# Optimization experiments

Hardware: AMD Instinct MI355X
Metric: run time of the kernel (lower is better)

Reference implementation:

```python
import jax, jax.numpy as jnp
import numpy as np

PAD = 0
NEG_INF = -1e30

B, P, Q, D = 32, 4096, 64, 128  # batch, passage len, question len, nhid


def setup_inputs() -> dict:
    key = jax.random.key(0)
    k1, k2, k3, k4, k5, k6 = jax.random.split(key, 6)
    return {
        "tensor_H": jax.random.normal(k1, (B, P, D), dtype=jnp.float32),
        "tensor_U": jax.random.normal(k2, (B, Q, D), dtype=jnp.float32),
        "M": jax.random.normal(k3, (B, P, D), dtype=jnp.float32),
        "sentence_word_rep": jax.random.randint(k4, (B, P), 0, 10000, dtype=jnp.int64),
        "W_attn": jax.random.normal(k5, (D, D), dtype=jnp.float32) / np.sqrt(D),
        "W_cls": jax.random.normal(k6, (5 * D, 2), dtype=jnp.float32) / np.sqrt(5 * D),
    }


def reference(tensor_H, tensor_U, M, sentence_word_rep, W_attn, W_cls):
    # Matrix attention (bilinear): S[b,p,q] = h_p^T W u_q  -> (B, P, Q)
    S = jnp.einsum("bpd,de,bqe->bpq", tensor_H, W_attn, tensor_U)
    # context-to-query: softmax over question axis, then bmm with U
    c2q = jnp.einsum("bpq,bqd->bpd", jax.nn.softmax(S, axis=2), tensor_U)
    # query-to-context: softmax over passage axis of row-max, weighted sum of H
    b_attn = jax.nn.softmax(jnp.max(S, axis=2), axis=-1)        # (B, P)
    q2c = jnp.einsum("bp,bpd->bd", b_attn, tensor_H)[:, None, :]  # (B, 1, D) broadcast over P
    # G = [H; c2q; H*c2q; H*q2c] -> (B, P, 4D); G_M = [G; M] -> (B, P, 5D)
    G_M = jnp.concatenate(
        [tensor_H, c2q, tensor_H * c2q, tensor_H * q2c, M], axis=2
    )
    # masked max-pool over passage positions (mask where token == PAD)
    pad_mask = (sentence_word_rep == PAD)[:, :, None]           # (B, P, 1)
    pooled = jnp.max(jnp.where(pad_mask, NEG_INF, G_M), axis=1)  # (B, 5D)
    # final linear classifier (no bias)
    return pooled @ W_cls                                        # (B, 2)
```

## Files before the change

kernel.cpp:

```cpp
#include <hip/hip_runtime.h>

#define B_ 32
#define P_ 4096
#define Q_ 64
#define D_ 128

#define PART_STRIDE 772
#define NCHUNK 32
#define CHUNK_ROWS 128
#define TWS_BYTES (96*16384)

typedef __attribute__((ext_vector_type(8))) short bf16x8;
typedef __attribute__((ext_vector_type(4))) float f32x4;

__device__ __forceinline__ unsigned int asu(float x) { return __float_as_uint(x); }
__device__ __forceinline__ float asf(unsigned int x) { return __uint_as_float(x); }

__global__ __launch_bounds__(256) void k_T(const float* __restrict__ U,
                                           const float* __restrict__ W,
                                           char* __restrict__ Tws) {
  __shared__ float Wl[128*132];
  __shared__ float Ul[8*128];
  const int b = blockIdx.x >> 3, qc = blockIdx.x & 7;
  const int t = threadIdx.x;
#pragma unroll
  for (int k = 0; k < 16; ++k) {
    int i = t*4 + k*1024;
    float4 wv = *(const float4*)(W + i);
    int d = i >> 7, e = i & 127;
    *(float4*)(&Wl[d*132 + e]) = wv;
  }
  {
    int i = t*4;
    int q = i >> 7, e = i & 127;
    *(float4*)(&Ul[q*128 + e]) =
        *(const float4*)(U + ((size_t)(b*Q_ + qc*8 + q))*D_ + e);
  }
  __syncthreads();
  const int d = t & 127, qhalf = t >> 7;
  char* Thi = Tws + b*16384;
  char* Tlo = Tws + 32*16384 + b*16384;
  char* Utl = Tws + 64*16384 + b*16384;
#pragma unroll
  for (int pass = 0; pass < 4; ++pass) {
    const int ql = pass*2 + qhalf;
    const int qg = qc*8 + ql;
    float acc = 0.f;
#pragma unroll
    for (int e = 0; e < 128; e += 4) {
      float4 wv = *(float4*)(&Wl[d*132 + e]);
      float4 uv = *(float4*)(&Ul[ql*128 + e]);
      acc += wv.x*uv.x + wv.y*uv.y + wv.z*uv.z + wv.w*uv.w;
    }
    unsigned int au = asu(acc);
    unsigned short hs = (unsigned short)(au >> 16);
    float lo = acc - asf(au & 0xFFFF0000u);
    unsigned short ls = (unsigned short)(asu(lo) >> 16);
    int ta = (qg*256 + 2*d) ^ ((qg & 7) << 4);
    *(unsigned short*)(Thi + ta) = hs;
    *(unsigned short*)(Tlo + ta) = ls;
    float uval = Ul[ql*128 + d];
    int ua = (d*128 + 2*qg) ^ ((d & 7) << 4);
    *(unsigned short*)(Utl + ua) = (unsigned short)(asu(uval) >> 16);
  }
}

__global__ __launch_bounds__(512, 4) void k_main(
    const float* __restrict__ H, const float* __restrict__ M,
    const int* __restrict__ tok, const char* __restrict__ Tws,
    float* __restrict__ part) {
  __shared__ __align__(16) char Thl[16384];
  __shared__ __align__(16) char Pl[16384];
  __shared__ __align__(16) float mrow[128];
  __shared__ __align__(16) float rzrow[128];
  __shared__ __align__(16) float prow[128];
  __shared__ __align__(16) float bm[128];
  __shared__ int tkl[128];

  const int bid = blockIdx.x;
  const int b = bid >> 5, chunk = bid & 31;
  const int t = threadIdx.x, wv = t >> 6, l = t & 63;
  const int r15 = l & 15, g4 = l >> 4;
  const char* Thi_g = Tws + b*16384;
  const char* Tlo_g = Tws + 32*16384 + b*16384;
  const char* Utl   = Tws + 64*16384 + b*16384;

  const int dd = wv*16 + r15;
  bf16x8 bu0 = *(const bf16x8*)(Utl + ((dd*128 +  0 + g4*16) ^ ((dd & 7) << 4)));
  bf16x8 bu1 = *(const bf16x8*)(Utl + ((dd*128 + 64 + g4*16) ^ ((dd & 7) << 4)));

  {
    const uint4* sh = (const uint4*)Thi_g;
    uint4* dh = (uint4*)Thl;
    dh[t]       = sh[t];
    dh[t + 512] = sh[t + 512];
  }
  if (t < 128) tkl[t] = tok[b*P_ + chunk*CHUNK_ROWS + t];
  __syncthreads();

  const int rowB = b*P_ + chunk*CHUNK_ROWS;

  {
    const int lrow0 = wv*16;
    const float* Arow = H + (size_t)(rowB + lrow0 + r15)*D_;
    f32x4 fA[4], fB[4];
#pragma unroll
    for (int ks = 0; ks < 4; ++ks) {
      const float* ap = Arow + ks*32 + g4*8;
      fA[ks] = *(const f32x4*)(ap);
      fB[ks] = *(const f32x4*)(ap + 4);
    }
    union { bf16x8 v; unsigned int u[4]; } Ah[4], Al[4];
#pragma unroll
    for (int ks = 0; ks < 4; ++ks) {
      unsigned int a0 = asu(fA[ks][0]), a1 = asu(fA[ks][1]),
                   a2 = asu(fA[ks][2]), a3 = asu(fA[ks][3]);
      unsigned int c0 = asu(fB[ks][0]), c1 = asu(fB[ks][1]),
                   c2 = asu(fB[ks][2]), c3 = asu(fB[ks][3]);
      Ah[ks].u[0] = (a1 & 0xFFFF0000u) | (a0 >> 16);
      Ah[ks].u[1] = (a3 & 0xFFFF0000u) | (a2 >> 16);
      Ah[ks].u[2] = (c1 & 0xFFFF0000u) | (c0 >> 16);
      Ah[ks].u[3] = (c3 & 0xFFFF0000u) | (c2 >> 16);
      float p0 = fA[ks][0] - asf(a0 & 0xFFFF0000u);
      float p1 = fA[ks][1] - asf(a1 & 0xFFFF0000u);
      float p2 = fA[ks][2] - asf(a2 & 0xFFFF0000u);
      float p3 = fA[ks][3] - asf(a3 & 0xFFFF0000u);
      float p4 = fB[ks][0] - asf(c0 & 0xFFFF0000u);
      float p5 = fB[ks][1] - asf(c1 & 0xFFFF0000u);
      float p6 = fB[ks][2] - asf(c2 & 0xFFFF0000u);
      float p7 = fB[ks][3] - asf(c3 & 0xFFFF0000u);
      Al[ks].u[0] = (asu(p1) & 0xFFFF0000u) | (asu(p0) >> 16);
      Al[ks].u[1] = (asu(p3) & 0xFFFF0000u) | (asu(p2) >> 16);
      Al[ks].u[2] = (asu(p5) & 0xFFFF0000u) | (asu(p4) >> 16);
      Al[ks].u[3] = (asu(p7) & 0xFFFF0000u) | (asu(p6) >> 16);
    }
    f32x4 sacc[4];
#pragma unroll
    for (int qt = 0; qt < 4; ++qt) sacc[qt] = (f32x4){0.f, 0.f, 0.f, 0.f};
#pragma unroll
    for (int ks = 0; ks < 4; ++ks) {
#pragma unroll
      for (int qt = 0; qt < 4; ++qt) {
        int q = qt*16 + r15;
        int off = (q*256 + ks*64 + g4*16) ^ ((q & 7) << 4);
        bf16x8 bh = *(const bf16x8*)(Thl + off);
        bf16x8 bl = *(const bf16x8*)(Tlo_g + off);
        sacc[qt] = __builtin_amdgcn_mfma_f32_16x16x32_bf16(Al[ks].v, bh, sacc[qt], 0, 0, 0);
        sacc[qt] = __builtin_amdgcn_mfma_f32_16x16x32_bf16(Ah[ks].v, bl, sacc[qt], 0, 0, 0);
        sacc[qt] = __builtin_amdgcn_mfma_f32_16x16x32_bf16(Ah[ks].v, bh, sacc[qt], 0, 0, 0);
      }
    }
    float m[4];
#pragma unroll
    for (int j = 0; j < 4; ++j)
      m[j] = fmaxf(fmaxf(sacc[0][j], sacc[1][j]), fmaxf(sacc[2][j], sacc[3][j]));
#pragma unroll
    for (int off = 1; off <= 8; off <<= 1)
#pragma unroll
      for (int j = 0; j < 4; ++j) m[j] = fmaxf(m[j], __shfl_xor(m[j], off));
    float Zp[4] = {0.f, 0.f, 0.f, 0.f};
#pragma unroll
    for (int qt = 0; qt < 4; ++qt)
#pragma unroll
      for (int j = 0; j < 4; ++j) {
        float e = __expf(sacc[qt][j] - m[j]);
        Zp[j] += e;
        int p = lrow0 + g4*4 + j, q = qt*16 + r15;
        int off = (p*128 + 2*q) ^ ((p & 7) << 4);
        *(unsigned short*)(Pl + off) = (unsigned short)(asu(e) >> 16);
      }
#pragma unroll
    for (int off = 1; off <= 8; off <<= 1)
#pragma unroll
      for (int j = 0; j < 4; ++j) Zp[j] += __shfl_xor(Zp[j], off);
    if (r15 == 0) {
#pragma unroll
      for (int j = 0; j < 4; ++j) {
        mrow[lrow0 + g4*4 + j]  = m[j];
        rzrow[lrow0 + g4*4 + j] = __builtin_amdgcn_rcpf(Zp[j]);
      }
    }
  }
  __syncthreads();

  float m0 = mrow[l], m1 = mrow[l + 64];
  float Lm = fmaxf(m0, m1);
#pragma unroll
  for (int off = 1; off <= 32; off <<= 1) Lm = fmaxf(Lm, __shfl_xor(Lm, off));
  float ssum = __expf(m0 - Lm) + __expf(m1 - Lm);
#pragma unroll
  for (int off = 1; off <= 32; off <<= 1) ssum += __shfl_xor(ssum, off);
  if (t < 128) {
    prow[t] = __expf(mrow[t] - Lm);
    bm[t]   = tkl[t] ? 0.f : -1.0e38f;
  }
  __syncthreads();

  float v = 0.f, xH = -3.0e38f, nH = 3.0e38f;
  float xC = -3.0e38f, xHC = -3.0e38f, xM = -3.0e38f;
#pragma unroll
  for (int rti = 0; rti < 8; ++rti) {
    const int rt = (rti + wv) & 7;
    f32x4 pv = (f32x4){0.f, 0.f, 0.f, 0.f};
    {
      int pr0 = rt*16 + r15;
      bf16x8 a0 = *(bf16x8*)(Pl + ((pr0*128 +  0 + g4*16) ^ ((r15 & 7) << 4)));
      bf16x8 a1 = *(bf16x8*)(Pl + ((pr0*128 + 64 + g4*16) ^ ((r15 & 7) << 4)));
      pv = __builtin_amdgcn_mfma_f32_16x16x32_bf16(a0, bu0, pv, 0, 0, 0);
      pv = __builtin_amdgcn_mfma_f32_16x16x32_bf16(a1, bu1, pv, 0, 0, 0);
    }
    const float* Hrow = H + (size_t)(rowB + rt*16 + g4*4)*D_ + dd;
    const float* Mrow = M + (size_t)(rowB + rt*16 + g4*4)*D_ + dd;
    const int rg = rt*16 + g4*4;
    f32x4 prw = *(const f32x4*)&prow[rg];
    f32x4 rzw = *(const f32x4*)&rzrow[rg];
    f32x4 bmw = *(const f32x4*)&bm[rg];
#pragma unroll
    for (int j = 0; j < 4; ++j) {
      const float bmax = bmw[j];
      const float bmin = -bmax;
      float h  = Hrow[(size_t)j*D_];
      float mv = Mrow[(size_t)j*D_];
      float c  = pv[j] * rzw[j];
      v   += prw[j]*h;
      xH   = fmaxf(xH,  h + bmax);
      nH   = fminf(nH,  h + bmin);
      xC   = fmaxf(xC,  c + bmax);
      xHC  = fmaxf(xHC, h*c + bmax);
      xM   = fmaxf(xM,  mv + bmax);
    }
  }
#pragma unroll
  for (int off = 16; off <= 32; off <<= 1) {
    v   += __shfl_xor(v, off);
    xH   = fmaxf(xH,  __shfl_xor(xH,  off));
    nH   = fminf(nH,  __shfl_xor(nH,  off));
    xC   = fmaxf(xC,  __shfl_xor(xC,  off));
    xHC  = fmaxf(xHC, __shfl_xor(xHC, off));
    xM   = fmaxf(xM,  __shfl_xor(xM,  off));
  }
  float* pp = part + (size_t)bid*PART_STRIDE;
  if (t == 0) { pp[0] = Lm; pp[1] = ssum; }
  if (g4 == 0) {
    pp[2 + dd]   = v;
    pp[130 + dd] = xH;
    pp[258 + dd] = nH;
    pp[386 + dd] = xC;
    pp[514 + dd] = xHC;
    pp[642 + dd] = xM;
  }
}

__global__ __launch_bounds__(128) void k_final(const float* __restrict__ part,
                                               const float* __restrict__ Wc,
                                               float* __restrict__ out) {
  __shared__ float pooled[640];
  __shared__ float r0s[2], r1s[2];
  const int b = blockIdx.x, t = threadIdx.x;
  const float* pb = part + (size_t)b*NCHUNK*PART_STRIDE;
  float L = -3.0e38f;
#pragma unroll
  for (int c = 0; c < NCHUNK; ++c) L = fmaxf(L, pb[c*PART_STRIDE]);
  float S = 0.f, V = 0.f;
  float mh = -3.0e38f, nh = 3.0e38f, mc = -3.0e38f, mhc = -3.0e38f, mm = -3.0e38f;
#pragma unroll
  for (int c = 0; c < NCHUNK; ++c) {
    const float* p = pb + c*PART_STRIDE;
    float e = __expf(p[0] - L);
    S += p[1]*e;
    V += p[2 + t]*e;
    mh  = fmaxf(mh,  p[130 + t]);
    nh  = fminf(nh,  p[258 + t]);
    mc  = fmaxf(mc,  p[386 + t]);
    mhc = fmaxf(mhc, p[514 + t]);
    mm  = fmaxf(mm,  p[642 + t]);
  }
  float q2c = V / S;
  pooled[t]       = mh;
  pooled[128 + t] = mc;
  pooled[256 + t] = mhc;
  pooled[384 + t] = (q2c >= 0.f) ? q2c*mh : q2c*nh;
  pooled[512 + t] = mm;
  __syncthreads();
  float a0 = 0.f, a1 = 0.f;
#pragma unroll
  for (int k = t; k < 640; k += 128) {
    float pv = pooled[k];
    a0 += pv*Wc[k*2 + 0];
    a1 += pv*Wc[k*2 + 1];
  }
#pragma unroll
  for (int off = 32; off; off >>= 1) {
    a0 += __shfl_xor(a0, off);
    a1 += __shfl_xor(a1, off);
  }
  if ((t & 63) == 0) { r0s[t >> 6] = a0; r1s[t >> 6] = a1; }
  __syncthreads();
  if (t == 0) {
    out[b*2 + 0] = r0s[0] + r0s[1];
    out[b*2 + 1] = r1s[0] + r1s[1];
  }
}

extern "C" void kernel_launch(void* const* d_in, const int* in_sizes, int n_in,
                              void* d_out, int out_size, void* d_ws, size_t ws_size,
                              hipStream_t stream) {
  const float* H   = (const float*)d_in[0];
  const float* U   = (const float*)d_in[1];
  const float* M   = (const float*)d_in[2];
  const int*   tok = (const int*)d_in[3];
  const float* Wa  = (const float*)d_in[4];
  const float* Wc  = (const float*)d_in[5];
  float* out = (float*)d_out;
  char* wsc = (char*)d_ws;
  char* Tws = wsc;
  float* part = (float*)(wsc + TWS_BYTES);

  hipLaunchKernelGGL(k_T,     dim3(256),        dim3(256), 0, stream, U, Wa, Tws);
  hipLaunchKernelGGL(k_main,  dim3(B_*NCHUNK),  dim3(512), 0, stream, H, M, tok, Tws, part);
  hipLaunchKernelGGL(k_final, dim3(B_),         dim3(128), 0, stream, part, Wc, out);
}
```

Baseline: 57.32 us.

## Split chunk epilogue: prefetch H for MFMA pass, vectorized H/M reduction pass

The per-chunk epilogue is split into two passes. The first prefetches all H values into registers before the MFMA loop and computes only the c2q-dependent maxima. The second re-reads H and M with coalesced 16-byte vector loads to compute the weighted sum and max/min pools, then reduces across warps through shared memory reused from the P buffer. This targets strided scalar global loads and load latency in the MFMA loop, at the cost of reading H twice, extra register pressure from the 32-entry buffer, and an extra shared-memory reduction with added barriers.

```diff
diff --git a/kernel.cpp b/kernel.cpp
--- a/kernel.cpp
+++ b/kernel.cpp
@@ -196,58 +196,106 @@
   }
   __syncthreads();
 
-  float v = 0.f, xH = -3.0e38f, nH = 3.0e38f;
-  float xC = -3.0e38f, xHC = -3.0e38f, xM = -3.0e38f;
-#pragma unroll
-  for (int rti = 0; rti < 8; ++rti) {
-    const int rt = (rti + wv) & 7;
-    f32x4 pv = (f32x4){0.f, 0.f, 0.f, 0.f};
-    {
-      int pr0 = rt*16 + r15;
-      bf16x8 a0 = *(bf16x8*)(Pl + ((pr0*128 +  0 + g4*16) ^ ((r15 & 7) << 4)));
-      bf16x8 a1 = *(bf16x8*)(Pl + ((pr0*128 + 64 + g4*16) ^ ((r15 & 7) << 4)));
-      pv = __builtin_amdgcn_mfma_f32_16x16x32_bf16(a0, bu0, pv, 0, 0, 0);
-      pv = __builtin_amdgcn_mfma_f32_16x16x32_bf16(a1, bu1, pv, 0, 0, 0);
-    }
-    const float* Hrow = H + (size_t)(rowB + rt*16 + g4*4)*D_ + dd;
-    const float* Mrow = M + (size_t)(rowB + rt*16 + g4*4)*D_ + dd;
-    const int rg = rt*16 + g4*4;
-    f32x4 prw = *(const f32x4*)&prow[rg];
-    f32x4 rzw = *(const f32x4*)&rzrow[rg];
-    f32x4 bmw = *(const f32x4*)&bm[rg];
-#pragma unroll
-    for (int j = 0; j < 4; ++j) {
-      const float bmax = bmw[j];
-      const float bmin = -bmax;
-      float h  = Hrow[(size_t)j*D_];
-      float mv = Mrow[(size_t)j*D_];
-      float c  = pv[j] * rzw[j];
-      v   += prw[j]*h;
-      xH   = fmaxf(xH,  h + bmax);
-      nH   = fminf(nH,  h + bmin);
-      xC   = fmaxf(xC,  c + bmax);
-      xHC  = fmaxf(xHC, h*c + bmax);
-      xM   = fmaxf(xM,  mv + bmax);
-    }
-  }
-#pragma unroll
-  for (int off = 16; off <= 32; off <<= 1) {
-    v   += __shfl_xor(v, off);
-    xH   = fmaxf(xH,  __shfl_xor(xH,  off));
-    nH   = fminf(nH,  __shfl_xor(nH,  off));
-    xC   = fmaxf(xC,  __shfl_xor(xC,  off));
-    xHC  = fmaxf(xHC, __shfl_xor(xHC, off));
-    xM   = fmaxf(xM,  __shfl_xor(xM,  off));
-  }
   float* pp = part + (size_t)bid*PART_STRIDE;
-  if (t == 0) { pp[0] = Lm; pp[1] = ssum; }
-  if (g4 == 0) {
-    pp[2 + dd]   = v;
-    pp[130 + dd] = xH;
-    pp[258 + dd] = nH;
-    pp[386 + dd] = xC;
-    pp[514 + dd] = xHC;
-    pp[642 + dd] = xM;
+
+  {
+    float hbuf[32];
+#pragma unroll
+    for (int rti = 0; rti < 8; ++rti) {
+      const int rt = (rti + wv) & 7;
+      const float* Hrow = H + (size_t)(rowB + rt*16 + g4*4)*D_ + dd;
+#pragma unroll
+      for (int j = 0; j < 4; ++j) hbuf[rti*4 + j] = Hrow[(size_t)j*D_];
+    }
+    __builtin_amdgcn_sched_barrier(0);
+
+    float xC = -3.0e38f, xHC = -3.0e38f;
+#pragma unroll
+    for (int rti = 0; rti < 8; ++rti) {
+      const int rt = (rti + wv) & 7;
+      f32x4 pv = (f32x4){0.f, 0.f, 0.f, 0.f};
+      {
+        int pr0 = rt*16 + r15;
+        bf16x8 a0 = *(bf16x8*)(Pl + ((pr0*128 +  0 + g4*16) ^ ((r15 & 7) << 4)));
+        bf16x8 a1 = *(bf16x8*)(Pl + ((pr0*128 + 64 + g4*16) ^ ((r15 & 7) << 4)));
+        pv = __builtin_amdgcn_mfma_f32_16x16x32_bf16(a0, bu0, pv, 0, 0, 0);
+        pv = __builtin_amdgcn_mfma_f32_16x16x32_bf16(a1, bu1, pv, 0, 0, 0);
+      }
+      const int rg = rt*16 + g4*4;
+      f32x4 rzw = *(const f32x4*)&rzrow[rg];
+      f32x4 bmw = *(const f32x4*)&bm[rg];
+#pragma unroll
+      for (int j = 0; j < 4; ++j) {
+        float c = pv[j] * rzw[j];
+        xC  = fmaxf(xC,  c + bmw[j]);
+        xHC = fmaxf(xHC, hbuf[rti*4 + j]*c + bmw[j]);
+      }
+    }
+#pragma unroll
+    for (int off = 16; off <= 32; off <<= 1) {
+      xC  = fmaxf(xC,  __shfl_xor(xC,  off));
+      xHC = fmaxf(xHC, __shfl_xor(xHC, off));
+    }
+    if (t == 0) { pp[0] = Lm; pp[1] = ssum; }
+    if (g4 == 0) {
+      pp[386 + dd] = xC;
+      pp[514 + dd] = xHC;
+    }
+  }
+  __syncthreads();
+
+  {
+    const int dq = t & 31, rg = t >> 5;
+    const float* Hs = H + (size_t)(rowB + rg)*D_ + dq*4;
+    const float* Ms = M + (size_t)(rowB + rg)*D_ + dq*4;
+    f32x4 v4  = (f32x4){0.f, 0.f, 0.f, 0.f};
+    f32x4 xH4 = (f32x4){-3.0e38f, -3.0e38f, -3.0e38f, -3.0e38f};
+    f32x4 nH4 = (f32x4){ 3.0e38f,  3.0e38f,  3.0e38f,  3.0e38f};
+    f32x4 xM4 = (f32x4){-3.0e38f, -3.0e38f, -3.0e38f, -3.0e38f};
+#pragma unroll
+    for (int s = 0; s < 8; ++s) {
+      const int row = rg + s*16;
+      f32x4 h4 = *(const f32x4*)(Hs + (size_t)s*16*D_);
+      f32x4 m4 = *(const f32x4*)(Ms + (size_t)s*16*D_);
+      float bmv = bm[row], prw = prow[row];
+#pragma unroll
+      for (int i = 0; i < 4; ++i) {
+        v4[i]  += prw*h4[i];
+        xH4[i]  = fmaxf(xH4[i], h4[i] + bmv);
+        nH4[i]  = fminf(nH4[i], h4[i] - bmv);
+        xM4[i]  = fmaxf(xM4[i], m4[i] + bmv);
+      }
+    }
+#pragma unroll
+    for (int i = 0; i < 4; ++i) {
+      v4[i]  += __shfl_xor(v4[i], 32);
+      xH4[i]  = fmaxf(xH4[i], __shfl_xor(xH4[i], 32));
+      nH4[i]  = fminf(nH4[i], __shfl_xor(nH4[i], 32));
+      xM4[i]  = fmaxf(xM4[i], __shfl_xor(xM4[i], 32));
+    }
+    if (l < 32) {
+      float* red = (float*)Pl;
+      *(f32x4*)&red[          wv*128 + dq*4] = v4;
+      *(f32x4*)&red[1024 +    wv*128 + dq*4] = xH4;
+      *(f32x4*)&red[2048 +    wv*128 + dq*4] = nH4;
+      *(f32x4*)&red[3072 +    wv*128 + dq*4] = xM4;
+    }
+  }
+  __syncthreads();
+  if (t < 128) {
+    const float* red = (const float*)Pl;
+    float v = 0.f, xh = -3.0e38f, nh = 3.0e38f, xm = -3.0e38f;
+#pragma unroll
+    for (int w = 0; w < 8; ++w) {
+      v  += red[w*128 + t];
+      xh  = fmaxf(xh, red[1024 + w*128 + t]);
+      nh  = fminf(nh, red[2048 + w*128 + t]);
+      xm  = fmaxf(xm, red[3072 + w*128 + t]);
+    }
+    pp[2 + t]   = v;
+    pp[130 + t] = xh;
+    pp[258 + t] = nh;
+    pp[642 + t] = xm;
   }
 }
 
```

Result: slower. 61.00 us (+6.4%).
